# Optimization experiments

Measured on AMD Instinct MI355X. Metric: run time of the kernel, lower is better.

Reference implementation:

```python
import jax, jax.numpy as jnp
import numpy as np

B, N, E, D, H = 128, 256, 1024, 128, 8
DK = D // H
NEG = -9e15

def _xavier(key, shape):
    lim = np.sqrt(6.0 / (shape[0] + shape[1]))
    return jax.random.uniform(key, shape, jnp.float32, -lim, lim)

def setup_inputs() -> dict:
    key = jax.random.key(0)
    ks = jax.random.split(key, 10)
    x = jax.random.normal(ks[0], (B, N, D), jnp.float32)
    mask = jax.random.randint(ks[1], (B, N), 0, 2) > 0
    mask = mask.at[:, 0].set(True)  # ensure no fully-masked molecule
    # unique (row, col) edges per molecule -> scatter .set matches torch index_put
    perm = jax.vmap(lambda k: jax.random.permutation(k, N * N)[:E])(jax.random.split(ks[2], B))
    edge_index = jnp.stack([perm // N, perm % N], axis=1).astype(jnp.int32)  # [B, 2, E]
    edge_attr = jax.random.normal(ks[3], (B, E, D), jnp.float32)
    return {
        "x": x, "mask": mask, "edge_index": edge_index, "edge_attr": edge_attr,
        "Wq": _xavier(ks[4], (D + 2, D)),
        "Wk": _xavier(ks[5], (D + 2, D)),
        "Wv": _xavier(ks[6], (D + 2, D)),
        "We_w": _xavier(ks[7], (D, D)),
        "We_b": jax.random.normal(ks[8], (D,), jnp.float32) * 0.02,
        "ln_g": jnp.ones((D,), jnp.float32),
        "ln_b": jnp.zeros((D,), jnp.float32),
    }

def reference(x, mask, edge_index, edge_attr, Wq, Wk, Wv, We_w, We_b, ln_g, ln_b):
    rows, cols = edge_index[:, 0, :], edge_index[:, 1, :]  # [B, E]
    # per-molecule degree features (torch_geometric.degree per row/col)
    deg = lambda idx: jax.vmap(lambda r: jnp.zeros((N,), x.dtype).at[r].add(1.0))(idx)
    deg_r, deg_c = deg(rows), deg(cols)
    x_new = jnp.concatenate([x, deg_r[..., None], deg_c[..., None]], axis=-1)  # [B,N,D+2]
    # edge bias: linear -> mean over features -> scatter into [B,N,N]
    edge_feats = (edge_attr @ We_w + We_b).mean(axis=-1)  # [B, E]
    edge_bias = jax.vmap(lambda r, c, f: jnp.zeros((N, N), x.dtype).at[r, c].set(f))(rows, cols, edge_feats)
    q = (x_new @ Wq).reshape(B, N, H, DK).transpose(0, 2, 1, 3)
    k = (x_new @ Wk).reshape(B, N, H, DK).transpose(0, 2, 1, 3)
    v = (x_new @ Wv).reshape(B, N, H, DK).transpose(0, 2, 1, 3)
    scores = jnp.einsum('bhqd,bhkd->bhqk', q, k) / np.sqrt(DK).astype(x.dtype)
    # mask keys first, then add edge bias (matches torch op order)
    scores = jnp.where(mask[:, None, None, :], scores, NEG) + edge_bias[:, None, :, :]
    attn = jax.nn.softmax(scores, axis=-1)  # dropout is identity in eval
    out = jnp.einsum('bhqk,bhkd->bhqd', attn, v).transpose(0, 2, 1, 3).reshape(B, N, D)
    out = out + x
    mu = out.mean(axis=-1, keepdims=True)
    var = out.var(axis=-1, keepdims=True)
    return (out - mu) / jnp.sqrt(var + 1e-6) * ln_g + ln_b
```

## Files before the change

### kernel.cpp

```cpp
#include <hip/hip_runtime.h>
#include <stdint.h>

#define NB 128
#define NN 256
#define NE 1024
#define ND 128
#define NH 8
#define NDK 16
#define NEGV -9.0e15f

typedef unsigned short u16;
typedef unsigned int u32;
typedef unsigned char u8;
typedef __attribute__((ext_vector_type(8))) short short8;
typedef __attribute__((ext_vector_type(4))) float float4v;
typedef __attribute__((ext_vector_type(2))) float f32x2;

__device__ __forceinline__ float bf2f(u16 u) { return __uint_as_float(((u32)u) << 16); }
__device__ __forceinline__ u16 f2bf(float f) {
    u32 u = __float_as_uint(f);
    u += 0x7fffu + ((u >> 16) & 1u);
    return (u16)(u >> 16);
}
__device__ __forceinline__ float ldf(const void* p, size_t i, int f32) {
    return f32 ? ((const float*)p)[i] : bf2f(((const u16*)p)[i]);
}
__device__ __forceinline__ void stf(void* p, size_t i, int f32, float v) {
    if (f32) ((float*)p)[i] = v;
    else ((u16*)p)[i] = f2bf(v);
}
__device__ __forceinline__ void unpack8(uint4 a, float* o) {
    o[0] = bf2f(a.x & 0xffff); o[1] = bf2f(a.x >> 16);
    o[2] = bf2f(a.y & 0xffff); o[3] = bf2f(a.y >> 16);
    o[4] = bf2f(a.z & 0xffff); o[5] = bf2f(a.z >> 16);
    o[6] = bf2f(a.w & 0xffff); o[7] = bf2f(a.w >> 16);
}
__device__ __forceinline__ f32x2 bfpair(u32 w) {
    return (f32x2){__uint_as_float(w << 16), __uint_as_float(w & 0xffff0000u)};
}
__device__ __forceinline__ u32 pk_bf(float a, float b) {
    return ((__float_as_uint(a) + 0x8000u) >> 16) |
           ((__float_as_uint(b) + 0x8000u) & 0xffff0000u);
}
union Pack8 { u16 u[8]; u32 w[4]; short8 v; };

__global__ __launch_bounds__(256) void k_detect(const u16* x16, const u8* m8, int* flags) {
    __shared__ u32 sev[256], sg1[256], smx[256];
    int tid = threadIdx.x;
    u32 ev = 0;
    for (int i = tid * 128; i < tid * 128 + 128; ++i) {
        u32 e = (x16[i] >> 7) & 0xffu;
        ev |= (e >= 0xC2u) ? 1u : 0u;
    }
    u32 g1 = 0, mx = 0;
    for (int i = 0; i < 16; ++i) {
        int idx = tid * 16 + i;
        u32 bv = m8[idx];
        if ((idx & 3) == 1) g1 |= bv;
        mx = mx > bv ? mx : bv;
    }
    sev[tid] = ev; sg1[tid] = g1; smx[tid] = mx;
    __syncthreads();
    for (int s = 128; s > 0; s >>= 1) {
        if (tid < s) {
            sev[tid] |= sev[tid + s];
            sg1[tid] |= sg1[tid + s];
            smx[tid] = smx[tid] > smx[tid + s] ? smx[tid] : smx[tid + s];
        }
        __syncthreads();
    }
    if (tid == 0) {
        flags[0] = sev[0] ? 1 : 0;
        flags[1] = (sg1[0] == 0) ? 4 : ((smx[0] <= 1u) ? 1 : 2);
    }
}

__global__ __launch_bounds__(64) void k_wmean(const void* Wew, const void* Web,
                                              const int* flags, float* wmean) {
    int k = blockIdx.x, lane = threadIdx.x;
    int f32 = flags[0];
    const void* src = (k < 128) ? Wew : Web;
    size_t base = (k < 128) ? (size_t)k * ND : 0;
    float s = ldf(src, base + lane, f32) + ldf(src, base + lane + 64, f32);
#pragma unroll
    for (int off = 32; off; off >>= 1) s += __shfl_xor(s, off, 64);
    if (lane == 0) wmean[k] = s * (1.0f / ND);
}

__global__ __launch_bounds__(256) void k_efeat(const void* ea, const float* wmean,
                                               const int* flags, float* featsE) {
    __shared__ __align__(16) float swm[132];
    int tid = threadIdx.x;
    int f32 = flags[0];
    if (tid <= ND) swm[tid] = wmean[tid];
    __syncthreads();
    int sub = tid & 15, grp = tid >> 4;
    size_t eidx = (size_t)blockIdx.x * 16 + grp;
    const float4* wv = (const float4*)&swm[sub * 8];
    float4 w0 = wv[0], w1 = wv[1];
    size_t base = eidx * ND + sub * 8;
    float part;
    if (f32) {
        const float4* p = (const float4*)((const float*)ea + base);
        float4 a0 = p[0], a1 = p[1];
        part = a0.x * w0.x + a0.y * w0.y + a0.z * w0.z + a0.w * w0.w +
               a1.x * w1.x + a1.y * w1.y + a1.z * w1.z + a1.w * w1.w;
    } else {
        uint4 a = *(const uint4*)((const u16*)ea + base);
        float xv[8];
        unpack8(a, xv);
        part = xv[0] * w0.x + xv[1] * w0.y + xv[2] * w0.z + xv[3] * w0.w +
               xv[4] * w1.x + xv[5] * w1.y + xv[6] * w1.z + xv[7] * w1.w;
    }
    part += __shfl_xor(part, 1);
    part += __shfl_xor(part, 2);
    part += __shfl_xor(part, 4);
    part += __shfl_xor(part, 8);
    if (sub == 0) featsE[eidx] = part + swm[ND];
}

__global__ __launch_bounds__(256) void k_csr(const int* ei, const float* featsE,
                                             float* degr, float* degc, int* rowstartG,
                                             u16* colsG, float* featsG) {
    __shared__ int cr[NN], cc[NN], offs[NN], rs[NN + 1];
    int b = blockIdx.x, tid = threadIdx.x;
    cr[tid] = 0; cc[tid] = 0;
    __syncthreads();
    const int* rows = ei + (size_t)b * 2 * NE;
    const int* cols = rows + NE;
    for (int e = tid; e < NE; e += 256) {
        atomicAdd(&cr[rows[e]], 1);
        atomicAdd(&cc[cols[e]], 1);
    }
    __syncthreads();
    degr[b * NN + tid] = (float)cr[tid];
    degc[b * NN + tid] = (float)cc[tid];
    if (tid == 0) {
        int a = 0;
        for (int n = 0; n < NN; ++n) { rs[n] = a; a += cr[n]; }
        rs[NN] = a;
    }
    __syncthreads();
    offs[tid] = rs[tid];
    rowstartG[b * (NN + 1) + tid] = rs[tid];
    if (tid == 0) rowstartG[b * (NN + 1) + NN] = rs[NN];
    __syncthreads();
    for (int e = tid; e < NE; e += 256) {
        int r = rows[e];
        int pos = atomicAdd(&offs[r], 1);
        colsG[(size_t)b * NE + pos] = (u16)cols[e];
        featsG[(size_t)b * NE + pos] = featsE[(size_t)b * NE + e];
    }
}

__global__ __launch_bounds__(64) void k_packB(const void* Wq, const void* Wk,
                                              const void* Wv, const int* flags, u16* WP) {
    int kT = blockIdx.x / 24, nT = blockIdx.x % 24;
    int lane = threadIdx.x;
    int col = lane & 15, quad = lane >> 4;
    int n = nT * 16 + col;
    int mat = n >> 7, nm = n & 127;
    const void* W = (mat == 0) ? Wq : (mat == 1) ? Wk : Wv;
    int f32 = flags[0];
    Pack8 c;
#pragma unroll
    for (int j = 0; j < 8; ++j) {
        int k = kT * 32 + quad * 8 + j;
        c.u[j] = (k < 130) ? f2bf(ldf(W, (size_t)k * ND + nm, f32)) : (u16)0;
    }
    *(short8*)(WP + ((size_t)(kT * 24 + nT) * 64 + lane) * 8) = c.v;
}

__global__ __launch_bounds__(256) void k_gemm(const void* x, const float* degr,
                                              const float* degc, const u16* WP,
                                              const int* flags, u16* qw, u16* kw,
                                              u16* vw, u16* vt) {
    int tid = threadIdx.x;
    int w = tid >> 6, lane = tid & 63;
    int quad = lane >> 4, col = lane & 15;
    int m0 = blockIdx.x * 64 + w * 16;
    int row = m0 + col;
    int f32 = flags[0];

    float4v acc[24];
#pragma unroll
    for (int t = 0; t < 24; ++t) acc[t] = (float4v){0.f, 0.f, 0.f, 0.f};

    const short8* wp = (const short8*)WP;
    for (int kT = 0; kT < 5; ++kT) {
        short8 a;
        if (kT < 4) {
            if (!f32) {
                a = *(const short8*)((const u16*)x + (size_t)row * ND + kT * 32 + quad * 8);
            } else {
                const float* xf = (const float*)x + (size_t)row * ND + kT * 32 + quad * 8;
                Pack8 c;
#pragma unroll
                for (int j = 0; j < 8; ++j) c.u[j] = f2bf(xf[j]);
                a = c.v;
            }
        } else {
            Pack8 c;
#pragma unroll
            for (int j = 0; j < 8; ++j) c.u[j] = 0;
            if (quad == 0) {
                c.u[0] = f2bf(degr[row]);
                c.u[1] = f2bf(degc[row]);
            }
            a = c.v;
        }
#pragma unroll
        for (int nT = 0; nT < 24; ++nT) {
            short8 bfr = wp[(size_t)(kT * 24 + nT) * 64 + lane];
            acc[nT] = __builtin_amdgcn_mfma_f32_16x16x32_bf16(a, bfr, acc[nT], 0, 0, 0);
        }
    }
    int bb = m0 >> 8;
    int nodebase = (m0 & 255) + quad * 4;
#pragma unroll
    for (int nT = 0; nT < 16; ++nT) {
        int h = nT & 7;
        u16* O = (nT < 8) ? qw : kw;
        float sc = (nT < 8) ? 0.25f : 1.0f;
        size_t base = ((size_t)bb * NH + h) * NN + nodebase;
#pragma unroll
        for (int reg = 0; reg < 4; ++reg)
            O[(base + reg) * NDK + col] = f2bf(acc[nT][reg] * sc);
    }
#pragma unroll
    for (int nT = 16; nT < 24; ++nT) {
        int h = nT - 16;
        size_t base = ((size_t)bb * NH + h) * NN + nodebase;
#pragma unroll
        for (int reg = 0; reg < 4; ++reg)
            vw[(base + reg) * NDK + col] = f2bf(acc[nT][reg]);
        u32 lo = (u32)f2bf(acc[nT][0]) | ((u32)f2bf(acc[nT][1]) << 16);
        u32 hi = (u32)f2bf(acc[nT][2]) | ((u32)f2bf(acc[nT][3]) << 16);
        *(uint2*)(vt + (((size_t)bb * NH + h) * NDK + col) * NN + nodebase) = make_uint2(lo, hi);
    }
}

__global__ __launch_bounds__(256) void k_attn(const u16* qg, const u16* kg,
                                              const u16* vw, const u16* vt,
                                              const void* mask, const int* flags,
                                              const int* rowstartG, const u16* colsG,
                                              const float* featsG, void* out) {
    __shared__ __align__(16) u16 Ks[NN][24];
    __shared__ __align__(16) u16 Vs[NDK][264];
    __shared__ __align__(16) float mb[NN];
    __shared__ __align__(16) float Of[NN * NDK];
    __shared__ float lbuf[NN];
    __shared__ u16 colsS[NE];
    __shared__ float featsS[NE];
    int h = blockIdx.x, b = blockIdx.y, tid = threadIdx.x;
    int wv = tid >> 6, lane = tid & 63;
    int col = lane & 15, g = lane >> 4;
    int f32 = flags[0], mw = flags[1];
    size_t hb = ((size_t)b * NH + h) * NN;
    {
        const uint4* src = (const uint4*)(kg + (hb + tid) * NDK);
        uint4 a0 = src[0], a1 = src[1];
        uint4* dst = (uint4*)&Ks[tid][0];
        dst[0] = a0; dst[1] = a1;
    }
    {
        int dk = tid >> 4, chunk = tid & 15;
        const uint4* src = (const uint4*)(vt + ((size_t)(b * NH + h) * NDK + dk) * NN + chunk * 16);
        uint4 a0 = src[0], a1 = src[1];
        uint4* dst = (uint4*)&Vs[dk][chunk * 16];
        dst[0] = a0; dst[1] = a1;
    }
    {
        size_t mi = (size_t)b * NN + tid;
        bool mv;
        if (mw == 4)      mv = ((const u32*)mask)[mi] != 0;
        else if (mw == 2) mv = ((const u16*)mask)[mi] != 0;
        else              mv = ((const u8*)mask)[mi] != 0;
        mb[tid] = mv ? 0.0f : NEGV;
    }
    for (int e = tid; e < NE; e += 256) {
        colsS[e] = colsG[(size_t)b * NE + e];
        featsS[e] = featsG[(size_t)b * NE + e];
    }
    short8 qf[4];
#pragma unroll
    for (int qt = 0; qt < 4; ++qt) {
        int qtabs = wv * 4 + qt;
        short8 qv = {0, 0, 0, 0, 0, 0, 0, 0};
        if (g < 2)
            qv = *(const short8*)(qg + (hb + qtabs * 16 + col) * NDK + 8 * g);
        qf[qt] = qv;
    }
    __syncthreads();

    float4v outv[4];
    float lpart[4];
#pragma unroll
    for (int qt = 0; qt < 4; ++qt) {
        outv[qt] = (float4v){0.f, 0.f, 0.f, 0.f};
        lpart[qt] = 0.f;
    }

    for (int kt = 0; kt < 16; ++kt) {
        short8 kf = {0, 0, 0, 0, 0, 0, 0, 0};
        if (g < 2) kf = *(const short8*)&Ks[kt * 16 + col][8 * g];
        Pack8 vv;
        {
            uint2 t2 = *(const uint2*)&Vs[col][kt * 16 + 4 * g];
            vv.w[0] = t2.x; vv.w[1] = t2.y; vv.w[2] = 0; vv.w[3] = 0;
        }
        float4 mb4 = *(const float4*)&mb[kt * 16 + 4 * g];
        float4v cin = (float4v){mb4.x, mb4.y, mb4.z, mb4.w};
#pragma unroll
        for (int qt = 0; qt < 4; ++qt) {
            float4v s4 = __builtin_amdgcn_mfma_f32_16x16x32_bf16(kf, qf[qt], cin, 0, 0, 0);
            float p0 = __expf(fminf(s4[0], 60.f));
            float p1 = __expf(fminf(s4[1], 60.f));
            float p2 = __expf(fminf(s4[2], 60.f));
            float p3 = __expf(fminf(s4[3], 60.f));
            lpart[qt] += (p0 + p1) + (p2 + p3);
            Pack8 pp;
            pp.w[0] = pk_bf(p0, p1);
            pp.w[1] = pk_bf(p2, p3);
            pp.w[2] = 0; pp.w[3] = 0;
            outv[qt] = __builtin_amdgcn_mfma_f32_16x16x32_bf16(pp.v, vv.v, outv[qt], 0, 0, 0);
        }
    }
#pragma unroll
    for (int qt = 0; qt < 4; ++qt) {
        float l = lpart[qt];
        l += __shfl_xor(l, 16);
        l += __shfl_xor(l, 32);
        if (g == 0) lbuf[(wv * 4 + qt) * 16 + col] = l;
        int q0 = (wv * 4 + qt) * 16 + 4 * g;
#pragma unroll
        for (int reg = 0; reg < 4; ++reg)
            Of[(q0 + reg) * NDK + col] = outv[qt][reg];
    }
    __syncthreads();

    float lfin = lbuf[tid];
    float* ofrow = &Of[tid * NDK];
    {
        const uint4* qp = (const uint4*)(qg + (hb + tid) * NDK);
        uint4 qa_ = qp[0], qb_ = qp[1];
        f32x2 qr[8];
        qr[0] = bfpair(qa_.x); qr[1] = bfpair(qa_.y);
        qr[2] = bfpair(qa_.z); qr[3] = bfpair(qa_.w);
        qr[4] = bfpair(qb_.x); qr[5] = bfpair(qb_.y);
        qr[6] = bfpair(qb_.z); qr[7] = bfpair(qb_.w);
        int e0 = rowstartG[b * (NN + 1) + tid];
        int e1 = rowstartG[b * (NN + 1) + tid + 1];
        for (int e = e0; e < e1; ++e) {
            int c = colsS[e];
            float f = featsS[e];
            const u32* kcw = (const u32*)&Ks[c][0];
            f32x2 s2 = qr[0] * bfpair(kcw[0]);
            s2 += qr[1] * bfpair(kcw[1]); s2 += qr[2] * bfpair(kcw[2]);
            s2 += qr[3] * bfpair(kcw[3]); s2 += qr[4] * bfpair(kcw[4]);
            s2 += qr[5] * bfpair(kcw[5]); s2 += qr[6] * bfpair(kcw[6]);
            s2 += qr[7] * bfpair(kcw[7]);
            float s = s2.x + s2.y + mb[c];
            float dl = __expf(fminf(s + f, 60.f)) - __expf(fminf(s, 60.f));
            lfin += dl;
            const uint4* vp = (const uint4*)(vw + (hb + c) * NDK);
            uint4 v0 = vp[0], v1 = vp[1];
            f32x2 d2 = (f32x2){dl, dl};
            f32x2* orow2 = (f32x2*)ofrow;
            orow2[0] += d2 * bfpair(v0.x); orow2[1] += d2 * bfpair(v0.y);
            orow2[2] += d2 * bfpair(v0.z); orow2[3] += d2 * bfpair(v0.w);
            orow2[4] += d2 * bfpair(v1.x); orow2[5] += d2 * bfpair(v1.y);
            orow2[6] += d2 * bfpair(v1.z); orow2[7] += d2 * bfpair(v1.w);
        }
    }
    float inv = 1.0f / lfin;
    size_t obase = ((size_t)(b * NN + tid)) * ND + h * NDK;
#pragma unroll
    for (int i = 0; i < NDK; ++i)
        stf(out, obase + i, f32, ofrow[i] * inv);
}

__global__ __launch_bounds__(256) void k_ln(void* out, const void* x, const void* g,
                                            const void* be, const int* flags) {
    int f32 = flags[0];
    int tid = threadIdx.x, wv = tid >> 6, lane = tid & 63;
    int row = blockIdx.x * 4 + wv;
    size_t base = (size_t)row * ND;
    float v0 = ldf(out, base + lane, f32) + ldf(x, base + lane, f32);
    float v1 = ldf(out, base + lane + 64, f32) + ldf(x, base + lane + 64, f32);
    float s = v0 + v1, ss = v0 * v0 + v1 * v1;
#pragma unroll
    for (int off = 32; off; off >>= 1) {
        s += __shfl_xor(s, off, 64);
        ss += __shfl_xor(ss, off, 64);
    }
    float mu = s * (1.0f / ND);
    float var = ss * (1.0f / ND) - mu * mu;
    float rs = rsqrtf(var + 1e-6f);
    float o0 = (v0 - mu) * rs * ldf(g, lane, f32) + ldf(be, lane, f32);
    float o1 = (v1 - mu) * rs * ldf(g, lane + 64, f32) + ldf(be, lane + 64, f32);
    stf(out, base + lane, f32, o0);
    stf(out, base + lane + 64, f32, o1);
}

extern "C" void kernel_launch(void* const* d_in, const int* in_sizes, int n_in,
                              void* d_out, int out_size, void* d_ws, size_t ws_size,
                              hipStream_t stream) {
    const void* x = d_in[0];
    const void* mask = d_in[1];
    const int* ei = (const int*)d_in[2];
    const void* ea = d_in[3];
    const void* Wq = d_in[4];
    const void* Wk = d_in[5];
    const void* Wv = d_in[6];
    const void* Wew = d_in[7];
    const void* Web = d_in[8];
    const void* lng = d_in[9];
    const void* lnb = d_in[10];

    char* ws = (char*)d_ws;
    size_t off = 0;
    int* flags = (int*)(ws + off);       off += 256;
    float* wmean = (float*)(ws + off);   off += 1024;
    float* degr = (float*)(ws + off);    off += (size_t)NB * NN * 4;
    float* degc = (float*)(ws + off);    off += (size_t)NB * NN * 4;
    int* rowstart = (int*)(ws + off);    off += (size_t)NB * (NN + 1) * 4 + 512;
    u16* colsG = (u16*)(ws + off);       off += (size_t)NB * NE * 2;
    float* featsG = (float*)(ws + off);  off += (size_t)NB * NE * 4;
    float* featsE = (float*)(ws + off);  off += (size_t)NB * NE * 4;
    u16* WP = (u16*)(ws + off);          off += (size_t)5 * 24 * 64 * 8 * 2;
    const size_t qkv_elems = (size_t)NB * NH * NN * NDK;
    u16* qw = (u16*)(ws + off);          off += qkv_elems * 2;
    u16* kw = (u16*)(ws + off);          off += qkv_elems * 2;
    u16* vw = (u16*)(ws + off);          off += qkv_elems * 2;
    u16* vt = (u16*)(ws + off);          off += qkv_elems * 2;

    k_detect<<<1, 256, 0, stream>>>((const u16*)x, (const u8*)mask, flags);
    k_wmean<<<129, 64, 0, stream>>>(Wew, Web, flags, wmean);
    k_efeat<<<(NB * NE) / 16, 256, 0, stream>>>(ea, wmean, flags, featsE);
    k_csr<<<NB, 256, 0, stream>>>(ei, featsE, degr, degc, rowstart, colsG, featsG);
    k_packB<<<120, 64, 0, stream>>>(Wq, Wk, Wv, flags, WP);
    k_gemm<<<(NB * NN) / 64, 256, 0, stream>>>(x, degr, degc, WP, flags, qw, kw, vw, vt);
    k_attn<<<dim3(NH, NB), 256, 0, stream>>>(qw, kw, vw, vt, mask, flags, rowstart,
                                             colsG, featsG, d_out);
    k_ln<<<(NB * NN) / 4, 256, 0, stream>>>(d_out, x, lng, lnb, flags);
}
```

Measured before the change: 219.6 us.

## Keep attention edge-correction accumulators in registers and trim k_attn shared memory

The edge-correction loop now accumulates the output row in registers instead of read-modify-writing shared memory. The per-molecule cols/feats staging into shared memory is removed; those values are read directly from global memory in the loop. The Of buffer is padded to stride 17 to avoid bank conflicts, the final output store is vectorised, and launch bounds request 4 blocks per CU. Together these aim to cut LDS traffic and footprint so more blocks fit per CU, at the cost of more register pressure and scattered global reads of edge data.

```diff
diff --git a/kernel.cpp b/kernel.cpp
--- a/kernel.cpp
+++ b/kernel.cpp
@@ -240,7 +240,7 @@
     }
 }
 
-__global__ __launch_bounds__(256) void k_attn(const u16* qg, const u16* kg,
+__global__ __launch_bounds__(256, 4) void k_attn(const u16* qg, const u16* kg,
                                               const u16* vw, const u16* vt,
                                               const void* mask, const int* flags,
                                               const int* rowstartG, const u16* colsG,
@@ -248,15 +248,15 @@
     __shared__ __align__(16) u16 Ks[NN][24];
     __shared__ __align__(16) u16 Vs[NDK][264];
     __shared__ __align__(16) float mb[NN];
-    __shared__ __align__(16) float Of[NN * NDK];
+    __shared__ __align__(16) float Of[NN * 17];
     __shared__ float lbuf[NN];
-    __shared__ u16 colsS[NE];
-    __shared__ float featsS[NE];
     int h = blockIdx.x, b = blockIdx.y, tid = threadIdx.x;
     int wv = tid >> 6, lane = tid & 63;
     int col = lane & 15, g = lane >> 4;
     int f32 = flags[0], mw = flags[1];
     size_t hb = ((size_t)b * NH + h) * NN;
+    int e0 = rowstartG[b * (NN + 1) + tid];
+    int e1 = rowstartG[b * (NN + 1) + tid + 1];
     {
         const uint4* src = (const uint4*)(kg + (hb + tid) * NDK);
         uint4 a0 = src[0], a1 = src[1];
@@ -277,10 +277,6 @@
         else if (mw == 2) mv = ((const u16*)mask)[mi] != 0;
         else              mv = ((const u8*)mask)[mi] != 0;
         mb[tid] = mv ? 0.0f : NEGV;
-    }
-    for (int e = tid; e < NE; e += 256) {
-        colsS[e] = colsG[(size_t)b * NE + e];
-        featsS[e] = featsG[(size_t)b * NE + e];
     }
     short8 qf[4];
 #pragma unroll
@@ -335,12 +331,15 @@
         int q0 = (wv * 4 + qt) * 16 + 4 * g;
 #pragma unroll
         for (int reg = 0; reg < 4; ++reg)
-            Of[(q0 + reg) * NDK + col] = outv[qt][reg];
+            Of[(q0 + reg) * 17 + col] = outv[qt][reg];
     }
     __syncthreads();
 
     float lfin = lbuf[tid];
-    float* ofrow = &Of[tid * NDK];
+    f32x2 r[8];
+#pragma unroll
+    for (int j = 0; j < 8; ++j)
+        r[j] = (f32x2){Of[tid * 17 + 2 * j], Of[tid * 17 + 2 * j + 1]};
     {
         const uint4* qp = (const uint4*)(qg + (hb + tid) * NDK);
         uint4 qa_ = qp[0], qb_ = qp[1];
@@ -349,11 +348,9 @@
         qr[2] = bfpair(qa_.z); qr[3] = bfpair(qa_.w);
         qr[4] = bfpair(qb_.x); qr[5] = bfpair(qb_.y);
         qr[6] = bfpair(qb_.z); qr[7] = bfpair(qb_.w);
-        int e0 = rowstartG[b * (NN + 1) + tid];
-        int e1 = rowstartG[b * (NN + 1) + tid + 1];
         for (int e = e0; e < e1; ++e) {
-            int c = colsS[e];
-            float f = featsS[e];
+            int c = colsG[(size_t)b * NE + e];
+            float f = featsG[(size_t)b * NE + e];
             const u32* kcw = (const u32*)&Ks[c][0];
             f32x2 s2 = qr[0] * bfpair(kcw[0]);
             s2 += qr[1] * bfpair(kcw[1]); s2 += qr[2] * bfpair(kcw[2]);
@@ -366,18 +363,36 @@
             const uint4* vp = (const uint4*)(vw + (hb + c) * NDK);
             uint4 v0 = vp[0], v1 = vp[1];
             f32x2 d2 = (f32x2){dl, dl};
-            f32x2* orow2 = (f32x2*)ofrow;
-            orow2[0] += d2 * bfpair(v0.x); orow2[1] += d2 * bfpair(v0.y);
-            orow2[2] += d2 * bfpair(v0.z); orow2[3] += d2 * bfpair(v0.w);
-            orow2[4] += d2 * bfpair(v1.x); orow2[5] += d2 * bfpair(v1.y);
-            orow2[6] += d2 * bfpair(v1.z); orow2[7] += d2 * bfpair(v1.w);
+            r[0] += d2 * bfpair(v0.x); r[1] += d2 * bfpair(v0.y);
+            r[2] += d2 * bfpair(v0.z); r[3] += d2 * bfpair(v0.w);
+            r[4] += d2 * bfpair(v1.x); r[5] += d2 * bfpair(v1.y);
+            r[6] += d2 * bfpair(v1.z); r[7] += d2 * bfpair(v1.w);
         }
     }
     float inv = 1.0f / lfin;
     size_t obase = ((size_t)(b * NN + tid)) * ND + h * NDK;
-#pragma unroll
-    for (int i = 0; i < NDK; ++i)
-        stf(out, obase + i, f32, ofrow[i] * inv);
+    if (f32) {
+        float4* op = (float4*)((float*)out + obase);
+#pragma unroll
+        for (int jj = 0; jj < 4; ++jj) {
+            float4 w;
+            w.x = r[2 * jj].x * inv;     w.y = r[2 * jj].y * inv;
+            w.z = r[2 * jj + 1].x * inv; w.w = r[2 * jj + 1].y * inv;
+            op[jj] = w;
+        }
+    } else {
+        u16* op = (u16*)out + obase;
+        Pack8 pa, pb;
+#pragma unroll
+        for (int jj = 0; jj < 4; ++jj) {
+            pa.u[2 * jj]     = f2bf(r[jj].x * inv);
+            pa.u[2 * jj + 1] = f2bf(r[jj].y * inv);
+            pb.u[2 * jj]     = f2bf(r[jj + 4].x * inv);
+            pb.u[2 * jj + 1] = f2bf(r[jj + 4].y * inv);
+        }
+        *(uint4*)op = *(uint4*)&pa.w[0];
+        *(uint4*)(op + 8) = *(uint4*)&pb.w[0];
+    }
 }
 
 __global__ __launch_bounds__(256) void k_ln(void* out, const void* x, const void* g,
```

New measurement: 208.8 us. 4.9% less time.
